# Performance work log

Measured on AMD Instinct MI355X. Metric: run time of the kernel, lower is better.

## Reference

```python
import jax, jax.numpy as jnp
import numpy as np

FEAT = 256
HEADS = 8
HD = FEAT // HEADS
POS = 128
NEG = 128
H = 128
W = 128
B = 8
NSLOT = 512
LN_EPS = 1e-5


def setup_inputs() -> dict:
    key = jax.random.key(0)
    ks = jax.random.split(key, 8)
    HW = H * W
    features = jax.random.normal(ks[0], (HW, B, FEAT), dtype=jnp.float32)
    pos_encodings = jax.random.normal(ks[1], (HW, B, FEAT), dtype=jnp.float32)
    slots = jax.random.normal(ks[2], (1, NSLOT, FEAT), dtype=jnp.float32)
    curio_maps = jax.random.uniform(ks[3], (NSLOT, H, W), dtype=jnp.float32)
    batch_idx = jax.random.randint(ks[4], (NSLOT,), 0, B, dtype=jnp.int32)
    # parameters (xavier-ish scale)
    in_proj_weight = jax.random.normal(ks[5], (3 * FEAT, FEAT), dtype=jnp.float32) * 0.05
    in_proj_bias = jnp.zeros((3 * FEAT,), dtype=jnp.float32)
    out_w = jax.random.normal(ks[6], (FEAT, FEAT), dtype=jnp.float32) * 0.05
    out_b = jnp.zeros((FEAT,), dtype=jnp.float32)
    ln_g = jnp.ones((FEAT,), dtype=jnp.float32)
    ln_b = jnp.zeros((FEAT,), dtype=jnp.float32)
    return {
        'slots': slots, 'features': features, 'pos_encodings': pos_encodings,
        'curio_maps': curio_maps, 'batch_idx': batch_idx,
        'in_proj_weight': in_proj_weight, 'in_proj_bias': in_proj_bias,
        'out_w': out_w, 'out_b': out_b, 'ln_g': ln_g, 'ln_b': ln_b,
        'max_mask_entries': 0,
    }


def _sample_feat_idx(curio_maps, max_mask_entries):
    # curio_maps: [NSLOT, H, W] -> feat_idx: [POS+NEG, NSLOT]
    HW = curio_maps.shape[1] * curio_maps.shape[2]
    flat = curio_maps.reshape(NSLOT, HW)
    sorted_idx = jnp.argsort(-flat, axis=1)  # descending
    pos_idx = sorted_idx[:, :POS]
    pool = sorted_idx[:, POS:HW - max_mask_entries] if max_mask_entries > 0 else sorted_idx[:, POS:]
    # deterministic stand-in for random.sample: evenly-strided negatives
    stride = pool.shape[1] // NEG
    neg_idx = pool[:, ::stride][:, :NEG]
    return jnp.concatenate([pos_idx, neg_idx], axis=1).T  # [S, NSLOT]


def _forward(slots, features, pos_encodings, curio_maps, batch_idx,
             in_proj_weight, in_proj_bias, out_w, out_b, ln_g, ln_b,
             max_mask_entries):
    feat_idx = _sample_feat_idx(curio_maps, max_mask_entries)  # [S, NSLOT]
    S = feat_idx.shape[0]
    qw, kw, vw = in_proj_weight[:FEAT], in_proj_weight[FEAT:2 * FEAT], in_proj_weight[2 * FEAT:]
    qb, kb, vb = in_proj_bias[:FEAT], in_proj_bias[FEAT:2 * FEAT], in_proj_bias[2 * FEAT:]
    scaling = float(HD) ** -0.5
    # sample_type == 'after': project full maps, then gather
    q = (jnp.einsum('bnf,gf->bng', slots, qw) + qb) * scaling       # [1, NSLOT, FEAT]
    k = jnp.einsum('pbf,gf->pbg', features + pos_encodings, kw) + kb  # [HW, B, FEAT]
    v = jnp.einsum('pbf,gf->pbg', features, vw) + vb                  # [HW, B, FEAT]
    kg = k[feat_idx, batch_idx[None, :], :]            # [S, NSLOT, FEAT]
    vg = v[feat_idx[:POS], batch_idx[None, :], :]      # [POS, NSLOT, FEAT]
    qh = q.reshape(NSLOT, HEADS, HD)
    kh = kg.reshape(S, NSLOT, HEADS, HD)
    vh = vg.reshape(POS, NSLOT, HEADS, HD)
    affinities = jnp.einsum('nhd,snhd->snh', qh, kh)   # [S, NSLOT, HEADS]
    attn = jax.nn.softmax(affinities[:POS], axis=0)    # softmax over positive samples
    attn_out = jnp.einsum('pnh,pnhd->nhd', attn, vh).reshape(1, NSLOT, FEAT)
    attn_out = jnp.einsum('bnf,gf->bng', attn_out, out_w) + out_b
    x = slots + attn_out  # dropout is identity in eval
    mu = jnp.mean(x, axis=-1, keepdims=True)
    var = jnp.var(x, axis=-1, keepdims=True)
    new_slots = (x - mu) / jnp.sqrt(var + LN_EPS) * ln_g + ln_b
    return new_slots, affinities


def reference(slots, features, pos_encodings, curio_maps, batch_idx,
              in_proj_weight, in_proj_bias, out_w, out_b, ln_g, ln_b,
              max_mask_entries):
    return _forward(slots, features, pos_encodings, curio_maps, batch_idx,
                    in_proj_weight, in_proj_bias, out_w, out_b, ln_g, ln_b,
                    max_mask_entries)
```

## Files before the change

kernel.cpp:

```cpp
#include <hip/hip_runtime.h>
#include <hip/hip_bf16.h>

#define FEAT 256
#define HEADS 8
#define HD 32
#define POSN 128
#define NEGN 128
#define HWN 16384
#define BN 8
#define NSLOT 512
#define S_TOT 256
#define LN_EPS 1e-5f
#define NBKT 4096
#define AFF_OFF (NSLOT*FEAT)

typedef float f32x4 __attribute__((ext_vector_type(4)));

__device__ __forceinline__ unsigned short bf16r(float x) {
    unsigned int u = __float_as_uint(x);
    u += 0x7FFFu + ((u >> 16) & 1u);
    return (unsigned short)(u >> 16);
}
__device__ __forceinline__ float bf16f(unsigned short h) {
    return __uint_as_float((unsigned int)h << 16);
}

__global__ __launch_bounds__(256) void k_sample_qkw(const float* __restrict__ curio,
                                                    const int* __restrict__ mme_p,
                                                    const float* __restrict__ slots,
                                                    const float* __restrict__ ipw,
                                                    const float* __restrict__ ipb,
                                                    int* __restrict__ fi_t,
                                                    float* __restrict__ qkw,
                                                    float* __restrict__ qkb)
{
    __shared__ unsigned int hist[NBKT];
    __shared__ uint16_t offs[NBKT];
    __shared__ uint16_t sidx[HWN];
    __shared__ unsigned int ssum[256];
    __shared__ float srow[FEAT];
    __shared__ float qrow[FEAT];
    int slot = blockIdx.x, t = threadIdx.x;
    const float* cm = curio + (size_t)slot * HWN;
    const f32x4* cm4 = (const f32x4*)cm;

    for (int i = t; i < NBKT; i += 256) hist[i] = 0;
    __syncthreads();

    unsigned int bkA[16], bkB[16];
#pragma unroll
    for (int j = 0; j < 16; j++) {
        f32x4 v = cm4[j * 256 + t];
        int b0 = (int)(v[0] * 4096.0f); b0 = b0 < 0 ? 0 : (b0 > NBKT-1 ? NBKT-1 : b0);
        int b1 = (int)(v[1] * 4096.0f); b1 = b1 < 0 ? 0 : (b1 > NBKT-1 ? NBKT-1 : b1);
        int b2 = (int)(v[2] * 4096.0f); b2 = b2 < 0 ? 0 : (b2 > NBKT-1 ? NBKT-1 : b2);
        int b3 = (int)(v[3] * 4096.0f); b3 = b3 < 0 ? 0 : (b3 > NBKT-1 ? NBKT-1 : b3);
        bkA[j] = (unsigned int)b0 | ((unsigned int)b1 << 16);
        bkB[j] = (unsigned int)b2 | ((unsigned int)b3 << 16);
        atomicAdd(&hist[b0], 1u); atomicAdd(&hist[b1], 1u);
        atomicAdd(&hist[b2], 1u); atomicAdd(&hist[b3], 1u);
    }
    __syncthreads();

    unsigned int lsum = 0;
    int base = t * 16;
    for (int j = 0; j < 16; j++) lsum += hist[NBKT-1 - (base + j)];
    ssum[t] = lsum; __syncthreads();
    for (int off = 1; off < 256; off <<= 1) {
        unsigned int v = (t >= off) ? ssum[t - off] : 0u;
        __syncthreads();
        ssum[t] += v;
        __syncthreads();
    }
    unsigned int run = ssum[t] - lsum;
    for (int j = 0; j < 16; j++) {
        int b = NBKT-1 - (base + j);
        offs[b] = (uint16_t)run;
        run += hist[b];
    }
    __syncthreads();
    for (int i = t; i < NBKT; i += 256) hist[i] = 0;
    __syncthreads();

#pragma unroll
    for (int j = 0; j < 16; j++) {
        int idx0 = (j * 256 + t) * 4;
        int b0 = (int)(bkA[j] & 0xFFFFu), b1 = (int)(bkA[j] >> 16);
        int b2 = (int)(bkB[j] & 0xFFFFu), b3 = (int)(bkB[j] >> 16);
        unsigned int p0 = (unsigned int)offs[b0] + atomicAdd(&hist[b0], 1u);
        sidx[p0] = (uint16_t)(idx0 + 0);
        unsigned int p1 = (unsigned int)offs[b1] + atomicAdd(&hist[b1], 1u);
        sidx[p1] = (uint16_t)(idx0 + 1);
        unsigned int p2 = (unsigned int)offs[b2] + atomicAdd(&hist[b2], 1u);
        sidx[p2] = (uint16_t)(idx0 + 2);
        unsigned int p3 = (unsigned int)offs[b3] + atomicAdd(&hist[b3], 1u);
        sidx[p3] = (uint16_t)(idx0 + 3);
    }
    __syncthreads();

    int mme = mme_p[0];
    int stride = (HWN - POSN - mme) / NEGN;
    int r = (t < POSN) ? t : (POSN + stride * (t - POSN));
    int lo = 0, hi = NBKT - 1;
    while (lo < hi) { int mid = (lo + hi) >> 1; if ((int)offs[mid] <= r) hi = mid; else lo = mid + 1; }
    int bkt = lo;
    int start = (int)offs[bkt];
    int cnt   = (int)hist[bkt];
    int rr = r - start;
    int besti = sidx[start + (rr < cnt ? rr : 0)];
    for (int j = 0; j < cnt; j++) {
        int ij = sidx[start + j];
        float vj = cm[ij];
        int rank = 0;
        for (int j2 = 0; j2 < cnt; j2++) {
            int i2 = sidx[start + j2];
            float v2 = cm[i2];
            if (v2 > vj || (v2 == vj && i2 < ij)) rank++;
        }
        if (rank == rr) { besti = ij; break; }
    }
    fi_t[slot * S_TOT + t] = besti;

    __syncthreads();
    srow[t] = slots[slot * FEAT + t];
    __syncthreads();
    {
        const float* qwrow = ipw + (size_t)t * FEAT;
        float acc = 0.f;
#pragma unroll 8
        for (int f = 0; f < FEAT; f++) acc += srow[f] * qwrow[f];
        const float scaling = 0.17677669529663687f;
        qrow[t] = (acc + ipb[t]) * scaling;
    }
    __syncthreads();
    if (t < HEADS) {
        float s = 0.f;
        for (int d = 0; d < HD; d++) s += qrow[t*HD + d] * ipb[FEAT + t*HD + d];
        qkb[slot * HEADS + t] = s;
    }
    const float* kw = ipw + FEAT * FEAT;
    for (int e = t; e < HEADS * FEAT; e += 256) {
        int h = e >> 8, f = e & 255;
        float s = 0.f;
#pragma unroll
        for (int d = 0; d < HD; d++) s += qrow[h*HD + d] * kw[(h*HD + d) * FEAT + f];
        qkw[(size_t)slot * (HEADS*FEAT) + e] = s;
    }
}

__global__ __launch_bounds__(512) void k_attn(const float* __restrict__ features,
                                              const float* __restrict__ pos_enc,
                                              const int* __restrict__ batch_idx,
                                              const int* __restrict__ fi_t,
                                              const float* __restrict__ qkw,
                                              const float* __restrict__ qkb,
                                              const float* __restrict__ slots,
                                              const float* __restrict__ ipw,
                                              const float* __restrict__ ipb,
                                              const float* __restrict__ out_w,
                                              const float* __restrict__ out_b,
                                              const float* __restrict__ ln_g,
                                              const float* __restrict__ ln_b,
                                              float* __restrict__ aff_out,
                                              float* __restrict__ out)
{
    __shared__ int   fi_l[S_TOT];
    __shared__ float qkb_l[HEADS];
    __shared__ __align__(16) float affP[POSN][8];
    __shared__ f32x4 wfp[4][HEADS][64];
    __shared__ f32x4 wf4[HEADS][64];
    __shared__ float aoh[512];
    __shared__ __align__(16) float ao_l[FEAT];
    __shared__ float xgh[512];
    __shared__ float r1[4], r2[4];

    int n = blockIdx.x, t = threadIdx.x, lane = t & 63, w = t >> 6;
    if (t < S_TOT) fi_l[t] = fi_t[n * S_TOT + t];
    if (t < HEADS) qkb_l[t] = qkb[n * HEADS + t];
    int b = batch_idx[n];

    const float* qk = qkw + (size_t)n * (HEADS*FEAT) + 4 * lane;
    f32x4 qw0 = *(const f32x4*)(qk + 0*FEAT);
    f32x4 qw1 = *(const f32x4*)(qk + 1*FEAT);
    f32x4 qw2 = *(const f32x4*)(qk + 2*FEAT);
    f32x4 qw3 = *(const f32x4*)(qk + 3*FEAT);
    f32x4 qw4 = *(const f32x4*)(qk + 4*FEAT);
    f32x4 qw5 = *(const f32x4*)(qk + 5*FEAT);
    f32x4 qw6 = *(const f32x4*)(qk + 6*FEAT);
    f32x4 qw7 = *(const f32x4*)(qk + 7*FEAT);
    __syncthreads();
    float qb = qkb_l[lane & 7];
    int b0 = lane & 1, b1 = (lane >> 1) & 1, b2 = (lane >> 2) & 1;

    auto dorow = [&](int p, f32x4 x, bool toLds) {
        float p0 = x[0]*qw0[0] + x[1]*qw0[1] + x[2]*qw0[2] + x[3]*qw0[3];
        float p1 = x[0]*qw1[0] + x[1]*qw1[1] + x[2]*qw1[2] + x[3]*qw1[3];
        float p2 = x[0]*qw2[0] + x[1]*qw2[1] + x[2]*qw2[2] + x[3]*qw2[3];
        float p3 = x[0]*qw3[0] + x[1]*qw3[1] + x[2]*qw3[2] + x[3]*qw3[3];
        float p4 = x[0]*qw4[0] + x[1]*qw4[1] + x[2]*qw4[2] + x[3]*qw4[3];
        float p5 = x[0]*qw5[0] + x[1]*qw5[1] + x[2]*qw5[2] + x[3]*qw5[3];
        float p6 = x[0]*qw6[0] + x[1]*qw6[1] + x[2]*qw6[2] + x[3]*qw6[3];
        float p7 = x[0]*qw7[0] + x[1]*qw7[1] + x[2]*qw7[2] + x[3]*qw7[3];
        float s0 = b0 ? p0 : p1, s1 = b0 ? p2 : p3, s2 = b0 ? p4 : p5, s3 = b0 ? p6 : p7;
        float a0 = (b0 ? p1 : p0) + __shfl_xor(s0, 1);
        float a1 = (b0 ? p3 : p2) + __shfl_xor(s1, 1);
        float a2 = (b0 ? p5 : p4) + __shfl_xor(s2, 1);
        float a3 = (b0 ? p7 : p6) + __shfl_xor(s3, 1);
        float u0 = b1 ? a0 : a1, u1 = b1 ? a2 : a3;
        float c0 = (b1 ? a1 : a0) + __shfl_xor(u0, 2);
        float c1 = (b1 ? a3 : a2) + __shfl_xor(u1, 2);
        float u2 = b2 ? c0 : c1;
        float d = (b2 ? c1 : c0) + __shfl_xor(u2, 4);
        d += __shfl_xor(d, 8);
        d += __shfl_xor(d, 16);
        d += __shfl_xor(d, 32);
        d += qb;
        if (lane < 8) {
            aff_out[(size_t)p * (NSLOT*HEADS) + n*HEADS + lane] = d;
            if (toLds) affP[p][lane] = d;
        }
    };

    auto rowaddr = [&](int s) {
        return ((size_t)fi_l[s] * BN + b) * FEAT + 4 * lane;
    };

    ushort4 cache[16];
    {
        size_t aA = rowaddr(w);
        size_t aB = rowaddr(w + 8);
        f32x4 fA = *(const f32x4*)(features + aA), gA = *(const f32x4*)(pos_enc + aA);
        f32x4 fB = *(const f32x4*)(features + aB), gB = *(const f32x4*)(pos_enc + aB);
#pragma unroll
        for (int i = 0; i < 16; i += 2) {
            f32x4 cf = fA, cg = gA;
            if (i + 2 < 16) {
                size_t nb = rowaddr(w + 8*(i+2));
                fA = *(const f32x4*)(features + nb); gA = *(const f32x4*)(pos_enc + nb);
            }
            { ushort4 pk; pk.x = bf16r(cf[0]); pk.y = bf16r(cf[1]);
              pk.z = bf16r(cf[2]); pk.w = bf16r(cf[3]); cache[i] = pk; }
            dorow(w + 8*i, cf + cg, true);
            f32x4 cf2 = fB, cg2 = gB;
            if (i + 3 < 16) {
                size_t nb = rowaddr(w + 8*(i+3));
                fB = *(const f32x4*)(features + nb); gB = *(const f32x4*)(pos_enc + nb);
            }
            { ushort4 pk; pk.x = bf16r(cf2[0]); pk.y = bf16r(cf2[1]);
              pk.z = bf16r(cf2[2]); pk.w = bf16r(cf2[3]); cache[i+1] = pk; }
            dorow(w + 8*(i+1), cf2 + cg2, true);
        }
    }
    __syncthreads();

    if (t < 256) {
        int h = t >> 5, l = t & 31;
        float v0 = affP[l][h], v1 = affP[l+32][h], v2 = affP[l+64][h], v3 = affP[l+96][h];
        float m = fmaxf(fmaxf(v0, v1), fmaxf(v2, v3));
        for (int off = 16; off > 0; off >>= 1) m = fmaxf(m, __shfl_xor(m, off, 32));
        float e0 = expf(v0 - m), e1 = expf(v1 - m), e2 = expf(v2 - m), e3 = expf(v3 - m);
        float s = e0 + e1 + e2 + e3;
        for (int off = 16; off > 0; off >>= 1) s += __shfl_xor(s, off, 32);
        float inv = 1.0f / s;
        affP[l][h] = e0*inv; affP[l+32][h] = e1*inv; affP[l+64][h] = e2*inv; affP[l+96][h] = e3*inv;
    }
    __syncthreads();

    f32x4 acc[8];
#pragma unroll
    for (int h = 0; h < 8; h++) acc[h] = (f32x4){0.f,0.f,0.f,0.f};
    {
        auto wstep = [&](int i) {
            int p = w + 8*i;
            ushort4 pk = cache[i];
            f32x4 xf;
            xf[0] = bf16f(pk.x); xf[1] = bf16f(pk.y);
            xf[2] = bf16f(pk.z); xf[3] = bf16f(pk.w);
            const f32x4* ap = (const f32x4*)&affP[p][0];
            f32x4 a03 = ap[0], a47 = ap[1];
            acc[0] += xf * a03[0];
            acc[1] += xf * a03[1];
            acc[2] += xf * a03[2];
            acc[3] += xf * a03[3];
            acc[4] += xf * a47[0];
            acc[5] += xf * a47[1];
            acc[6] += xf * a47[2];
            acc[7] += xf * a47[3];
        };
        size_t aA = rowaddr(POSN + w);
        size_t aB = rowaddr(POSN + w + 8);
        f32x4 fA = *(const f32x4*)(features + aA), gA = *(const f32x4*)(pos_enc + aA);
        f32x4 fB = *(const f32x4*)(features + aB), gB = *(const f32x4*)(pos_enc + aB);
#pragma unroll
        for (int i = 0; i < 16; i += 2) {
            f32x4 cf = fA, cg = gA;
            if (i + 2 < 16) {
                size_t nb = rowaddr(POSN + w + 8*(i+2));
                fA = *(const f32x4*)(features + nb); gA = *(const f32x4*)(pos_enc + nb);
            }
            wstep(i);
            dorow(POSN + w + 8*i, cf + cg, false);
            f32x4 cf2 = fB, cg2 = gB;
            if (i + 3 < 16) {
                size_t nb = rowaddr(POSN + w + 8*(i+3));
                fB = *(const f32x4*)(features + nb); gB = *(const f32x4*)(pos_enc + nb);
            }
            wstep(i+1);
            dorow(POSN + w + 8*(i+1), cf2 + cg2, false);
        }
    }
    if (w < 4) {
#pragma unroll
        for (int h = 0; h < 8; h++) wfp[w][h][lane] = acc[h];
    }
    __syncthreads();
    if (w >= 4) {
#pragma unroll
        for (int h = 0; h < 8; h++) wfp[w-4][h][lane] += acc[h];
    }
    __syncthreads();
    {
        int h = t >> 6, q2 = t & 63;
        f32x4 s = wfp[0][h][q2] + wfp[1][h][q2] + wfp[2][h][q2] + wfp[3][h][q2];
        wf4[h][q2] = s;
    }
    __syncthreads();

    {
        int g = t & 255, half = t >> 8;
        const float* vwrow = ipw + (size_t)(2*FEAT + g) * FEAT + half*128;
        const f32x4* wfv = &wf4[g >> 5][half*32];
        float s = 0.f;
#pragma unroll 8
        for (int f4i = 0; f4i < 32; f4i++) {
            f32x4 wv = *(const f32x4*)(vwrow + 4*f4i);
            f32x4 y = wfv[f4i];
            s += wv[0]*y[0] + wv[1]*y[1] + wv[2]*y[2] + wv[3]*y[3];
        }
        aoh[t] = s;
    }
    __syncthreads();
    if (t < 256) ao_l[t] = aoh[t] + aoh[t + 256] + ipb[2*FEAT + t];
    __syncthreads();

    {
        int g = t & 255, half = t >> 8;
        const float* owrow = out_w + (size_t)g * FEAT + half*128;
        const f32x4* av = (const f32x4*)&ao_l[half*128];
        float s = 0.f;
#pragma unroll 8
        for (int f4i = 0; f4i < 32; f4i++) {
            f32x4 wv = *(const f32x4*)(owrow + 4*f4i);
            f32x4 y = av[f4i];
            s += wv[0]*y[0] + wv[1]*y[1] + wv[2]*y[2] + wv[3]*y[3];
        }
        xgh[t] = s;
    }
    __syncthreads();

    float xg = 0.f;
    if (t < 256) {
        xg = xgh[t] + xgh[t + 256] + out_b[t] + slots[n * FEAT + t];
        float s1 = xg, s2 = xg * xg;
        for (int off = 32; off > 0; off >>= 1) {
            s1 += __shfl_xor(s1, off);
            s2 += __shfl_xor(s2, off);
        }
        if ((t & 63) == 0) { r1[t >> 6] = s1; r2[t >> 6] = s2; }
    }
    __syncthreads();
    if (t < 256) {
        float sum1 = r1[0] + r1[1] + r1[2] + r1[3];
        float sum2 = r2[0] + r2[1] + r2[2] + r2[3];
        float mu  = sum1 * (1.0f / FEAT);
        float var = sum2 * (1.0f / FEAT) - mu * mu;
        float nrm = (xg - mu) * rsqrtf(var + LN_EPS);
        out[n * FEAT + t] = nrm * ln_g[t] + ln_b[t];
    }
}

extern "C" void kernel_launch(void* const* d_in, const int* in_sizes, int n_in,
                              void* d_out, int out_size, void* d_ws, size_t ws_size,
                              hipStream_t stream)
{
    (void)in_sizes; (void)n_in; (void)out_size; (void)ws_size;
    const float* slots    = (const float*)d_in[0];
    const float* features = (const float*)d_in[1];
    const float* pos_enc  = (const float*)d_in[2];
    const float* curio    = (const float*)d_in[3];
    const int*   batch_idx= (const int*)d_in[4];
    const float* ipw      = (const float*)d_in[5];
    const float* ipb      = (const float*)d_in[6];
    const float* out_w    = (const float*)d_in[7];
    const float* out_b    = (const float*)d_in[8];
    const float* ln_g     = (const float*)d_in[9];
    const float* ln_b     = (const float*)d_in[10];
    const int*   mme      = (const int*)d_in[11];
    float* out = (float*)d_out;

    char* ws = (char*)d_ws;
    int*   fi_t = (int*)ws;
    float* qkw  = (float*)(ws + (512 << 10));
    float* qkb  = (float*)(ws + (512 << 10) + (4 << 20));
    float* aff  = out + AFF_OFF;

    hipLaunchKernelGGL(k_sample_qkw, dim3(NSLOT), dim3(256), 0, stream,
                       curio, mme, slots, ipw, ipb, fi_t, qkw, qkb);
    hipLaunchKernelGGL(k_attn, dim3(NSLOT), dim3(512), 0, stream,
                       features, pos_enc, batch_idx, fi_t, qkw, qkb, slots, ipw, ipb,
                       out_w, out_b, ln_g, ln_b, aff, out);
}
```

Measured before the change: 132.2 us.

## Split attention kernel into gather/reduce kernel and separate projection+LayerNorm kernel

```diff
diff --git a/kernel.cpp b/kernel.cpp
--- a/kernel.cpp
+++ b/kernel.cpp
@@ -148,31 +148,19 @@
     }
 }
 
-__global__ __launch_bounds__(512) void k_attn(const float* __restrict__ features,
-                                              const float* __restrict__ pos_enc,
-                                              const int* __restrict__ batch_idx,
-                                              const int* __restrict__ fi_t,
-                                              const float* __restrict__ qkw,
-                                              const float* __restrict__ qkb,
-                                              const float* __restrict__ slots,
-                                              const float* __restrict__ ipw,
-                                              const float* __restrict__ ipb,
-                                              const float* __restrict__ out_w,
-                                              const float* __restrict__ out_b,
-                                              const float* __restrict__ ln_g,
-                                              const float* __restrict__ ln_b,
-                                              float* __restrict__ aff_out,
-                                              float* __restrict__ out)
+__global__ __launch_bounds__(512) void k_attn_mem(const float* __restrict__ features,
+                                                  const float* __restrict__ pos_enc,
+                                                  const int* __restrict__ batch_idx,
+                                                  const int* __restrict__ fi_t,
+                                                  const float* __restrict__ qkw,
+                                                  const float* __restrict__ qkb,
+                                                  float* __restrict__ aff_out,
+                                                  f32x4* __restrict__ wf_g)
 {
     __shared__ int   fi_l[S_TOT];
     __shared__ float qkb_l[HEADS];
     __shared__ __align__(16) float affP[POSN][8];
     __shared__ f32x4 wfp[4][HEADS][64];
-    __shared__ f32x4 wf4[HEADS][64];
-    __shared__ float aoh[512];
-    __shared__ __align__(16) float ao_l[FEAT];
-    __shared__ float xgh[512];
-    __shared__ float r1[4], r2[4];
 
     int n = blockIdx.x, t = threadIdx.x, lane = t & 63, w = t >> 6;
     if (t < S_TOT) fi_l[t] = fi_t[n * S_TOT + t];
@@ -251,6 +239,14 @@
             dorow(w + 8*(i+1), cf2 + cg2, true);
         }
     }
+
+    f32x4 fA, gA, fB, gB;
+    {
+        size_t aA = rowaddr(POSN + w);
+        size_t aB = rowaddr(POSN + w + 8);
+        fA = *(const f32x4*)(features + aA); gA = *(const f32x4*)(pos_enc + aA);
+        fB = *(const f32x4*)(features + aB); gB = *(const f32x4*)(pos_enc + aB);
+    }
     __syncthreads();
 
     if (t < 256) {
@@ -287,10 +283,6 @@
             acc[6] += xf * a47[2];
             acc[7] += xf * a47[3];
         };
-        size_t aA = rowaddr(POSN + w);
-        size_t aB = rowaddr(POSN + w + 8);
-        f32x4 fA = *(const f32x4*)(features + aA), gA = *(const f32x4*)(pos_enc + aA);
-        f32x4 fB = *(const f32x4*)(features + aB), gB = *(const f32x4*)(pos_enc + aB);
 #pragma unroll
         for (int i = 0; i < 16; i += 2) {
             f32x4 cf = fA, cg = gA;
@@ -322,7 +314,30 @@
     {
         int h = t >> 6, q2 = t & 63;
         f32x4 s = wfp[0][h][q2] + wfp[1][h][q2] + wfp[2][h][q2] + wfp[3][h][q2];
-        wf4[h][q2] = s;
+        wf_g[(size_t)n * 512 + t] = s;
+    }
+}
+
+__global__ __launch_bounds__(512) void k_proj(const f32x4* __restrict__ wf_g,
+                                              const float* __restrict__ slots,
+                                              const float* __restrict__ ipw,
+                                              const float* __restrict__ ipb,
+                                              const float* __restrict__ out_w,
+                                              const float* __restrict__ out_b,
+                                              const float* __restrict__ ln_g,
+                                              const float* __restrict__ ln_b,
+                                              float* __restrict__ out)
+{
+    __shared__ f32x4 wf4[HEADS][64];
+    __shared__ float aoh[512];
+    __shared__ __align__(16) float ao_l[FEAT];
+    __shared__ float xgh[512];
+    __shared__ float r1[4], r2[4];
+
+    int n = blockIdx.x, t = threadIdx.x;
+    {
+        int h = t >> 6, q2 = t & 63;
+        wf4[h][q2] = wf_g[(size_t)n * 512 + t];
     }
     __syncthreads();
 
@@ -399,14 +414,19 @@
     float* out = (float*)d_out;
 
     char* ws = (char*)d_ws;
+    const size_t OFF_QKW = 512u << 10;
+    const size_t OFF_QKB = OFF_QKW + (4u << 20);
+    const size_t OFF_WF  = OFF_QKB + (64u << 10);
     int*   fi_t = (int*)ws;
-    float* qkw  = (float*)(ws + (512 << 10));
-    float* qkb  = (float*)(ws + (512 << 10) + (4 << 20));
+    float* qkw  = (float*)(ws + OFF_QKW);
+    float* qkb  = (float*)(ws + OFF_QKB);
+    f32x4* wf_g = (f32x4*)(ws + OFF_WF);
     float* aff  = out + AFF_OFF;
 
     hipLaunchKernelGGL(k_sample_qkw, dim3(NSLOT), dim3(256), 0, stream,
                        curio, mme, slots, ipw, ipb, fi_t, qkw, qkb);
-    hipLaunchKernelGGL(k_attn, dim3(NSLOT), dim3(512), 0, stream,
-                       features, pos_enc, batch_idx, fi_t, qkw, qkb, slots, ipw, ipb,
-                       out_w, out_b, ln_g, ln_b, aff, out);
-}
+    hipLaunchKernelGGL(k_attn_mem, dim3(NSLOT), dim3(512), 0, stream,
+                       features, pos_enc, batch_idx, fi_t, qkw, qkb, aff, wf_g);
+    hipLaunchKernelGGL(k_proj, dim3(NSLOT), dim3(512), 0, stream,
+                       wf_g, slots, ipw, ipb, out_w, out_b, ln_g, ln_b, out);
+}
```

After: 132.9 us. No clear change (+0.5%).

## Fuse sampling/QK-weight kernel into attention kernel with shared LDS union

Applied to the files above, without the earlier changes.

```diff
diff --git a/kernel.cpp b/kernel.cpp
--- a/kernel.cpp
+++ b/kernel.cpp
@@ -25,106 +25,129 @@
     return __uint_as_float((unsigned int)h << 16);
 }
 
-__global__ __launch_bounds__(256) void k_sample_qkw(const float* __restrict__ curio,
-                                                    const int* __restrict__ mme_p,
-                                                    const float* __restrict__ slots,
-                                                    const float* __restrict__ ipw,
-                                                    const float* __restrict__ ipb,
-                                                    int* __restrict__ fi_t,
-                                                    float* __restrict__ qkw,
-                                                    float* __restrict__ qkb)
+__global__ __launch_bounds__(512) void k_fused(const float* __restrict__ curio,
+                                               const int* __restrict__ mme_p,
+                                               const float* __restrict__ slots,
+                                               const float* __restrict__ ipw,
+                                               const float* __restrict__ ipb,
+                                               const int* __restrict__ batch_idx,
+                                               const float* __restrict__ features,
+                                               const float* __restrict__ pos_enc,
+                                               const float* __restrict__ out_w,
+                                               const float* __restrict__ out_b,
+                                               const float* __restrict__ ln_g,
+                                               const float* __restrict__ ln_b,
+                                               float* __restrict__ aff_out,
+                                               float* __restrict__ out)
 {
-    __shared__ unsigned int hist[NBKT];
-    __shared__ uint16_t offs[NBKT];
-    __shared__ uint16_t sidx[HWN];
-    __shared__ unsigned int ssum[256];
+    __shared__ __align__(16) char U[59392];
+    unsigned int* hist = (unsigned int*)U;
+    uint16_t*     offs = (uint16_t*)(U + 16384);
+    uint16_t*     sidx = (uint16_t*)(U + 24576);
+    unsigned int* ssum = (unsigned int*)(U + 57344);
+    float (*affP)[8] = (float(*)[8])U;
+    f32x4 (*wfp)[HEADS][64] = (f32x4(*)[HEADS][64])(U + 4096);
+    f32x4 (*wf4)[64] = (f32x4(*)[64])(U + 36864);
+    float* aoh  = (float*)(U + 45056);
+    float* ao_l = (float*)(U + 47104);
+    float* xgh  = (float*)(U + 48128);
+    float* rr12 = (float*)(U + 50176);
+    __shared__ int   fi_l[S_TOT];
+    __shared__ float qkwL[HEADS*FEAT];
+    __shared__ float qkb_l[HEADS];
     __shared__ float srow[FEAT];
     __shared__ float qrow[FEAT];
-    int slot = blockIdx.x, t = threadIdx.x;
-    const float* cm = curio + (size_t)slot * HWN;
+
+    int n = blockIdx.x, t = threadIdx.x, lane = t & 63, w = t >> 6;
+    const float* cm = curio + (size_t)n * HWN;
     const f32x4* cm4 = (const f32x4*)cm;
-
-    for (int i = t; i < NBKT; i += 256) hist[i] = 0;
-    __syncthreads();
-
-    unsigned int bkA[16], bkB[16];
-#pragma unroll
-    for (int j = 0; j < 16; j++) {
-        f32x4 v = cm4[j * 256 + t];
-        int b0 = (int)(v[0] * 4096.0f); b0 = b0 < 0 ? 0 : (b0 > NBKT-1 ? NBKT-1 : b0);
-        int b1 = (int)(v[1] * 4096.0f); b1 = b1 < 0 ? 0 : (b1 > NBKT-1 ? NBKT-1 : b1);
-        int b2 = (int)(v[2] * 4096.0f); b2 = b2 < 0 ? 0 : (b2 > NBKT-1 ? NBKT-1 : b2);
-        int b3 = (int)(v[3] * 4096.0f); b3 = b3 < 0 ? 0 : (b3 > NBKT-1 ? NBKT-1 : b3);
-        bkA[j] = (unsigned int)b0 | ((unsigned int)b1 << 16);
-        bkB[j] = (unsigned int)b2 | ((unsigned int)b3 << 16);
-        atomicAdd(&hist[b0], 1u); atomicAdd(&hist[b1], 1u);
-        atomicAdd(&hist[b2], 1u); atomicAdd(&hist[b3], 1u);
-    }
-    __syncthreads();
-
-    unsigned int lsum = 0;
-    int base = t * 16;
-    for (int j = 0; j < 16; j++) lsum += hist[NBKT-1 - (base + j)];
-    ssum[t] = lsum; __syncthreads();
-    for (int off = 1; off < 256; off <<= 1) {
-        unsigned int v = (t >= off) ? ssum[t - off] : 0u;
-        __syncthreads();
-        ssum[t] += v;
-        __syncthreads();
-    }
-    unsigned int run = ssum[t] - lsum;
-    for (int j = 0; j < 16; j++) {
-        int b = NBKT-1 - (base + j);
-        offs[b] = (uint16_t)run;
-        run += hist[b];
-    }
-    __syncthreads();
-    for (int i = t; i < NBKT; i += 256) hist[i] = 0;
-    __syncthreads();
-
-#pragma unroll
-    for (int j = 0; j < 16; j++) {
-        int idx0 = (j * 256 + t) * 4;
-        int b0 = (int)(bkA[j] & 0xFFFFu), b1 = (int)(bkA[j] >> 16);
-        int b2 = (int)(bkB[j] & 0xFFFFu), b3 = (int)(bkB[j] >> 16);
-        unsigned int p0 = (unsigned int)offs[b0] + atomicAdd(&hist[b0], 1u);
+    int b = batch_idx[n];
+
+    for (int i = t; i < NBKT; i += 512) hist[i] = 0;
+    __syncthreads();
+
+    unsigned int bkA[8], bkB[8];
+#pragma unroll
+    for (int j = 0; j < 8; j++) {
+        f32x4 v = cm4[j * 512 + t];
+        int c0 = (int)(v[0] * 4096.0f); c0 = c0 < 0 ? 0 : (c0 > NBKT-1 ? NBKT-1 : c0);
+        int c1 = (int)(v[1] * 4096.0f); c1 = c1 < 0 ? 0 : (c1 > NBKT-1 ? NBKT-1 : c1);
+        int c2 = (int)(v[2] * 4096.0f); c2 = c2 < 0 ? 0 : (c2 > NBKT-1 ? NBKT-1 : c2);
+        int c3 = (int)(v[3] * 4096.0f); c3 = c3 < 0 ? 0 : (c3 > NBKT-1 ? NBKT-1 : c3);
+        bkA[j] = (unsigned int)c0 | ((unsigned int)c1 << 16);
+        bkB[j] = (unsigned int)c2 | ((unsigned int)c3 << 16);
+        atomicAdd(&hist[c0], 1u); atomicAdd(&hist[c1], 1u);
+        atomicAdd(&hist[c2], 1u); atomicAdd(&hist[c3], 1u);
+    }
+    __syncthreads();
+
+    {
+        unsigned int lsum = 0;
+        int base = t * 8;
+        for (int j = 0; j < 8; j++) lsum += hist[NBKT-1 - (base + j)];
+        ssum[t] = lsum; __syncthreads();
+        for (int off = 1; off < 512; off <<= 1) {
+            unsigned int v = (t >= off) ? ssum[t - off] : 0u;
+            __syncthreads();
+            ssum[t] += v;
+            __syncthreads();
+        }
+        unsigned int run = ssum[t] - lsum;
+        for (int j = 0; j < 8; j++) {
+            int bb = NBKT-1 - (base + j);
+            offs[bb] = (uint16_t)run;
+            run += hist[bb];
+        }
+    }
+    __syncthreads();
+    for (int i = t; i < NBKT; i += 512) hist[i] = 0;
+    __syncthreads();
+
+#pragma unroll
+    for (int j = 0; j < 8; j++) {
+        int idx0 = (j * 512 + t) * 4;
+        int c0 = (int)(bkA[j] & 0xFFFFu), c1 = (int)(bkA[j] >> 16);
+        int c2 = (int)(bkB[j] & 0xFFFFu), c3 = (int)(bkB[j] >> 16);
+        unsigned int p0 = (unsigned int)offs[c0] + atomicAdd(&hist[c0], 1u);
         sidx[p0] = (uint16_t)(idx0 + 0);
-        unsigned int p1 = (unsigned int)offs[b1] + atomicAdd(&hist[b1], 1u);
+        unsigned int p1 = (unsigned int)offs[c1] + atomicAdd(&hist[c1], 1u);
         sidx[p1] = (uint16_t)(idx0 + 1);
-        unsigned int p2 = (unsigned int)offs[b2] + atomicAdd(&hist[b2], 1u);
+        unsigned int p2 = (unsigned int)offs[c2] + atomicAdd(&hist[c2], 1u);
         sidx[p2] = (uint16_t)(idx0 + 2);
-        unsigned int p3 = (unsigned int)offs[b3] + atomicAdd(&hist[b3], 1u);
+        unsigned int p3 = (unsigned int)offs[c3] + atomicAdd(&hist[c3], 1u);
         sidx[p3] = (uint16_t)(idx0 + 3);
     }
     __syncthreads();
 
-    int mme = mme_p[0];
-    int stride = (HWN - POSN - mme) / NEGN;
-    int r = (t < POSN) ? t : (POSN + stride * (t - POSN));
-    int lo = 0, hi = NBKT - 1;
-    while (lo < hi) { int mid = (lo + hi) >> 1; if ((int)offs[mid] <= r) hi = mid; else lo = mid + 1; }
-    int bkt = lo;
-    int start = (int)offs[bkt];
-    int cnt   = (int)hist[bkt];
-    int rr = r - start;
-    int besti = sidx[start + (rr < cnt ? rr : 0)];
-    for (int j = 0; j < cnt; j++) {
-        int ij = sidx[start + j];
-        float vj = cm[ij];
-        int rank = 0;
-        for (int j2 = 0; j2 < cnt; j2++) {
-            int i2 = sidx[start + j2];
-            float v2 = cm[i2];
-            if (v2 > vj || (v2 == vj && i2 < ij)) rank++;
-        }
-        if (rank == rr) { besti = ij; break; }
-    }
-    fi_t[slot * S_TOT + t] = besti;
-
-    __syncthreads();
-    srow[t] = slots[slot * FEAT + t];
-    __syncthreads();
-    {
+    if (t < S_TOT) {
+        int mme = mme_p[0];
+        int stride = (HWN - POSN - mme) / NEGN;
+        int r = (t < POSN) ? t : (POSN + stride * (t - POSN));
+        int lo = 0, hi = NBKT - 1;
+        while (lo < hi) { int mid = (lo + hi) >> 1; if ((int)offs[mid] <= r) hi = mid; else lo = mid + 1; }
+        int bkt = lo;
+        int start = (int)offs[bkt];
+        int cnt   = (int)hist[bkt];
+        int rsel  = r - start;
+        int besti = sidx[start + (rsel < cnt ? rsel : 0)];
+        for (int j = 0; j < cnt; j++) {
+            int ij = sidx[start + j];
+            float vj = cm[ij];
+            int rank = 0;
+            for (int j2 = 0; j2 < cnt; j2++) {
+                int i2 = sidx[start + j2];
+                float v2 = cm[i2];
+                if (v2 > vj || (v2 == vj && i2 < ij)) rank++;
+            }
+            if (rank == rsel) { besti = ij; break; }
+        }
+        fi_l[t] = besti;
+    }
+
+    __syncthreads();
+    if (t < FEAT) srow[t] = slots[n * FEAT + t];
+    __syncthreads();
+    if (t < FEAT) {
         const float* qwrow = ipw + (size_t)t * FEAT;
         float acc = 0.f;
 #pragma unroll 8
@@ -136,61 +159,30 @@
     if (t < HEADS) {
         float s = 0.f;
         for (int d = 0; d < HD; d++) s += qrow[t*HD + d] * ipb[FEAT + t*HD + d];
-        qkb[slot * HEADS + t] = s;
-    }
-    const float* kw = ipw + FEAT * FEAT;
-    for (int e = t; e < HEADS * FEAT; e += 256) {
-        int h = e >> 8, f = e & 255;
-        float s = 0.f;
-#pragma unroll
-        for (int d = 0; d < HD; d++) s += qrow[h*HD + d] * kw[(h*HD + d) * FEAT + f];
-        qkw[(size_t)slot * (HEADS*FEAT) + e] = s;
-    }
-}
-
-__global__ __launch_bounds__(512) void k_attn(const float* __restrict__ features,
-                                              const float* __restrict__ pos_enc,
-                                              const int* __restrict__ batch_idx,
-                                              const int* __restrict__ fi_t,
-                                              const float* __restrict__ qkw,
-                                              const float* __restrict__ qkb,
-                                              const float* __restrict__ slots,
-                                              const float* __restrict__ ipw,
-                                              const float* __restrict__ ipb,
-                                              const float* __restrict__ out_w,
-                                              const float* __restrict__ out_b,
-                                              const float* __restrict__ ln_g,
-                                              const float* __restrict__ ln_b,
-                                              float* __restrict__ aff_out,
-                                              float* __restrict__ out)
-{
-    __shared__ int   fi_l[S_TOT];
-    __shared__ float qkb_l[HEADS];
-    __shared__ __align__(16) float affP[POSN][8];
-    __shared__ f32x4 wfp[4][HEADS][64];
-    __shared__ f32x4 wf4[HEADS][64];
-    __shared__ float aoh[512];
-    __shared__ __align__(16) float ao_l[FEAT];
-    __shared__ float xgh[512];
-    __shared__ float r1[4], r2[4];
-
-    int n = blockIdx.x, t = threadIdx.x, lane = t & 63, w = t >> 6;
-    if (t < S_TOT) fi_l[t] = fi_t[n * S_TOT + t];
-    if (t < HEADS) qkb_l[t] = qkb[n * HEADS + t];
-    int b = batch_idx[n];
-
-    const float* qk = qkw + (size_t)n * (HEADS*FEAT) + 4 * lane;
-    f32x4 qw0 = *(const f32x4*)(qk + 0*FEAT);
-    f32x4 qw1 = *(const f32x4*)(qk + 1*FEAT);
-    f32x4 qw2 = *(const f32x4*)(qk + 2*FEAT);
-    f32x4 qw3 = *(const f32x4*)(qk + 3*FEAT);
-    f32x4 qw4 = *(const f32x4*)(qk + 4*FEAT);
-    f32x4 qw5 = *(const f32x4*)(qk + 5*FEAT);
-    f32x4 qw6 = *(const f32x4*)(qk + 6*FEAT);
-    f32x4 qw7 = *(const f32x4*)(qk + 7*FEAT);
-    __syncthreads();
+        qkb_l[t] = s;
+    }
+    {
+        const float* kw = ipw + FEAT * FEAT;
+        for (int e = t; e < HEADS * FEAT; e += 512) {
+            int h = e >> 8, f = e & 255;
+            float s = 0.f;
+#pragma unroll
+            for (int d = 0; d < HD; d++) s += qrow[h*HD + d] * kw[(h*HD + d) * FEAT + f];
+            qkwL[e] = s;
+        }
+    }
+    __syncthreads();
+
+    f32x4 qw0 = *(const f32x4*)&qkwL[0*FEAT + 4*lane];
+    f32x4 qw1 = *(const f32x4*)&qkwL[1*FEAT + 4*lane];
+    f32x4 qw2 = *(const f32x4*)&qkwL[2*FEAT + 4*lane];
+    f32x4 qw3 = *(const f32x4*)&qkwL[3*FEAT + 4*lane];
+    f32x4 qw4 = *(const f32x4*)&qkwL[4*FEAT + 4*lane];
+    f32x4 qw5 = *(const f32x4*)&qkwL[5*FEAT + 4*lane];
+    f32x4 qw6 = *(const f32x4*)&qkwL[6*FEAT + 4*lane];
+    f32x4 qw7 = *(const f32x4*)&qkwL[7*FEAT + 4*lane];
     float qb = qkb_l[lane & 7];
-    int b0 = lane & 1, b1 = (lane >> 1) & 1, b2 = (lane >> 2) & 1;
+    int e0 = lane & 1, e1 = (lane >> 1) & 1, e2 = (lane >> 2) & 1;
 
     auto dorow = [&](int p, f32x4 x, bool toLds) {
         float p0 = x[0]*qw0[0] + x[1]*qw0[1] + x[2]*qw0[2] + x[3]*qw0[3];
@@ -201,16 +193,16 @@
         float p5 = x[0]*qw5[0] + x[1]*qw5[1] + x[2]*qw5[2] + x[3]*qw5[3];
         float p6 = x[0]*qw6[0] + x[1]*qw6[1] + x[2]*qw6[2] + x[3]*qw6[3];
         float p7 = x[0]*qw7[0] + x[1]*qw7[1] + x[2]*qw7[2] + x[3]*qw7[3];
-        float s0 = b0 ? p0 : p1, s1 = b0 ? p2 : p3, s2 = b0 ? p4 : p5, s3 = b0 ? p6 : p7;
-        float a0 = (b0 ? p1 : p0) + __shfl_xor(s0, 1);
-        float a1 = (b0 ? p3 : p2) + __shfl_xor(s1, 1);
-        float a2 = (b0 ? p5 : p4) + __shfl_xor(s2, 1);
-        float a3 = (b0 ? p7 : p6) + __shfl_xor(s3, 1);
-        float u0 = b1 ? a0 : a1, u1 = b1 ? a2 : a3;
-        float c0 = (b1 ? a1 : a0) + __shfl_xor(u0, 2);
-        float c1 = (b1 ? a3 : a2) + __shfl_xor(u1, 2);
-        float u2 = b2 ? c0 : c1;
-        float d = (b2 ? c1 : c0) + __shfl_xor(u2, 4);
+        float s0 = e0 ? p0 : p1, s1 = e0 ? p2 : p3, s2 = e0 ? p4 : p5, s3 = e0 ? p6 : p7;
+        float a0 = (e0 ? p1 : p0) + __shfl_xor(s0, 1);
+        float a1 = (e0 ? p3 : p2) + __shfl_xor(s1, 1);
+        float a2 = (e0 ? p5 : p4) + __shfl_xor(s2, 1);
+        float a3 = (e0 ? p7 : p6) + __shfl_xor(s3, 1);
+        float u0 = e1 ? a0 : a1, u1 = e1 ? a2 : a3;
+        float c0 = (e1 ? a1 : a0) + __shfl_xor(u0, 2);
+        float c1 = (e1 ? a3 : a2) + __shfl_xor(u1, 2);
+        float u2 = e2 ? c0 : c1;
+        float d = (e2 ? c1 : c0) + __shfl_xor(u2, 4);
         d += __shfl_xor(d, 8);
         d += __shfl_xor(d, 16);
         d += __shfl_xor(d, 32);
@@ -251,6 +243,14 @@
             dorow(w + 8*(i+1), cf2 + cg2, true);
         }
     }
+
+    f32x4 fA, gA, fB, gB;
+    {
+        size_t aA = rowaddr(POSN + w);
+        size_t aB = rowaddr(POSN + w + 8);
+        fA = *(const f32x4*)(features + aA); gA = *(const f32x4*)(pos_enc + aA);
+        fB = *(const f32x4*)(features + aB); gB = *(const f32x4*)(pos_enc + aB);
+    }
     __syncthreads();
 
     if (t < 256) {
@@ -258,11 +258,11 @@
         float v0 = affP[l][h], v1 = affP[l+32][h], v2 = affP[l+64][h], v3 = affP[l+96][h];
         float m = fmaxf(fmaxf(v0, v1), fmaxf(v2, v3));
         for (int off = 16; off > 0; off >>= 1) m = fmaxf(m, __shfl_xor(m, off, 32));
-        float e0 = expf(v0 - m), e1 = expf(v1 - m), e2 = expf(v2 - m), e3 = expf(v3 - m);
-        float s = e0 + e1 + e2 + e3;
+        float ex0 = expf(v0 - m), ex1 = expf(v1 - m), ex2 = expf(v2 - m), ex3 = expf(v3 - m);
+        float s = ex0 + ex1 + ex2 + ex3;
         for (int off = 16; off > 0; off >>= 1) s += __shfl_xor(s, off, 32);
         float inv = 1.0f / s;
-        affP[l][h] = e0*inv; affP[l+32][h] = e1*inv; affP[l+64][h] = e2*inv; affP[l+96][h] = e3*inv;
+        affP[l][h] = ex0*inv; affP[l+32][h] = ex1*inv; affP[l+64][h] = ex2*inv; affP[l+96][h] = ex3*inv;
     }
     __syncthreads();
 
@@ -287,10 +287,6 @@
             acc[6] += xf * a47[2];
             acc[7] += xf * a47[3];
         };
-        size_t aA = rowaddr(POSN + w);
-        size_t aB = rowaddr(POSN + w + 8);
-        f32x4 fA = *(const f32x4*)(features + aA), gA = *(const f32x4*)(pos_enc + aA);
-        f32x4 fB = *(const f32x4*)(features + aB), gB = *(const f32x4*)(pos_enc + aB);
 #pragma unroll
         for (int i = 0; i < 16; i += 2) {
             f32x4 cf = fA, cg = gA;
@@ -321,8 +317,7 @@
     __syncthreads();
     {
         int h = t >> 6, q2 = t & 63;
-        f32x4 s = wfp[0][h][q2] + wfp[1][h][q2] + wfp[2][h][q2] + wfp[3][h][q2];
-        wf4[h][q2] = s;
+        wf4[h][q2] = wfp[0][h][q2] + wfp[1][h][q2] + wfp[2][h][q2] + wfp[3][h][q2];
     }
     __syncthreads();
 
@@ -342,7 +337,6 @@
     __syncthreads();
     if (t < 256) ao_l[t] = aoh[t] + aoh[t + 256] + ipb[2*FEAT + t];
     __syncthreads();
-
     {
         int g = t & 255, half = t >> 8;
         const float* owrow = out_w + (size_t)g * FEAT + half*128;
@@ -366,12 +360,12 @@
             s1 += __shfl_xor(s1, off);
             s2 += __shfl_xor(s2, off);
         }
-        if ((t & 63) == 0) { r1[t >> 6] = s1; r2[t >> 6] = s2; }
+        if ((t & 63) == 0) { rr12[t >> 6] = s1; rr12[4 + (t >> 6)] = s2; }
     }
     __syncthreads();
     if (t < 256) {
-        float sum1 = r1[0] + r1[1] + r1[2] + r1[3];
-        float sum2 = r2[0] + r2[1] + r2[2] + r2[3];
+        float sum1 = rr12[0] + rr12[1] + rr12[2] + rr12[3];
+        float sum2 = rr12[4] + rr12[5] + rr12[6] + rr12[7];
         float mu  = sum1 * (1.0f / FEAT);
         float var = sum2 * (1.0f / FEAT) - mu * mu;
         float nrm = (xg - mu) * rsqrtf(var + LN_EPS);
@@ -383,7 +377,7 @@
                               void* d_out, int out_size, void* d_ws, size_t ws_size,
                               hipStream_t stream)
 {
-    (void)in_sizes; (void)n_in; (void)out_size; (void)ws_size;
+    (void)in_sizes; (void)n_in; (void)out_size; (void)d_ws; (void)ws_size;
     const float* slots    = (const float*)d_in[0];
     const float* features = (const float*)d_in[1];
     const float* pos_enc  = (const float*)d_in[2];
@@ -397,16 +391,9 @@
     const float* ln_b     = (const float*)d_in[10];
     const int*   mme      = (const int*)d_in[11];
     float* out = (float*)d_out;
-
-    char* ws = (char*)d_ws;
-    int*   fi_t = (int*)ws;
-    float* qkw  = (float*)(ws + (512 << 10));
-    float* qkb  = (float*)(ws + (512 << 10) + (4 << 20));
-    float* aff  = out + AFF_OFF;
-
-    hipLaunchKernelGGL(k_sample_qkw, dim3(NSLOT), dim3(256), 0, stream,
-                       curio, mme, slots, ipw, ipb, fi_t, qkw, qkb);
-    hipLaunchKernelGGL(k_attn, dim3(NSLOT), dim3(512), 0, stream,
-                       features, pos_enc, batch_idx, fi_t, qkw, qkb, slots, ipw, ipb,
+    float* aff = out + AFF_OFF;
+
+    hipLaunchKernelGGL(k_fused, dim3(NSLOT), dim3(512), 0, stream,
+                       curio, mme, slots, ipw, ipb, batch_idx, features, pos_enc,
                        out_w, out_b, ln_g, ln_b, aff, out);
 }
```

Result: slower. 140.5 us (+6.2%).

## Coalesce matvecs via wave-cooperative dot8w and prefetch negative rows before softmax

Applied to the files above, without the earlier changes.

```diff
diff --git a/kernel.cpp b/kernel.cpp
--- a/kernel.cpp
+++ b/kernel.cpp
@@ -23,6 +23,42 @@
 }
 __device__ __forceinline__ float bf16f(unsigned short h) {
     return __uint_as_float((unsigned int)h << 16);
+}
+
+__device__ __forceinline__ float dot8w(const float* __restrict__ Wrows,
+                                       f32x4 x, int e0, int e1, int e2, int lane)
+{
+    const float* p = Wrows + 4 * lane;
+    f32x4 w0 = *(const f32x4*)(p + 0*FEAT);
+    f32x4 w1 = *(const f32x4*)(p + 1*FEAT);
+    f32x4 w2 = *(const f32x4*)(p + 2*FEAT);
+    f32x4 w3 = *(const f32x4*)(p + 3*FEAT);
+    f32x4 w4 = *(const f32x4*)(p + 4*FEAT);
+    f32x4 w5 = *(const f32x4*)(p + 5*FEAT);
+    f32x4 w6 = *(const f32x4*)(p + 6*FEAT);
+    f32x4 w7 = *(const f32x4*)(p + 7*FEAT);
+    float p0 = x[0]*w0[0] + x[1]*w0[1] + x[2]*w0[2] + x[3]*w0[3];
+    float p1 = x[0]*w1[0] + x[1]*w1[1] + x[2]*w1[2] + x[3]*w1[3];
+    float p2 = x[0]*w2[0] + x[1]*w2[1] + x[2]*w2[2] + x[3]*w2[3];
+    float p3 = x[0]*w3[0] + x[1]*w3[1] + x[2]*w3[2] + x[3]*w3[3];
+    float p4 = x[0]*w4[0] + x[1]*w4[1] + x[2]*w4[2] + x[3]*w4[3];
+    float p5 = x[0]*w5[0] + x[1]*w5[1] + x[2]*w5[2] + x[3]*w5[3];
+    float p6 = x[0]*w6[0] + x[1]*w6[1] + x[2]*w6[2] + x[3]*w6[3];
+    float p7 = x[0]*w7[0] + x[1]*w7[1] + x[2]*w7[2] + x[3]*w7[3];
+    float s0 = e0 ? p0 : p1, s1 = e0 ? p2 : p3, s2 = e0 ? p4 : p5, s3 = e0 ? p6 : p7;
+    float a0 = (e0 ? p1 : p0) + __shfl_xor(s0, 1);
+    float a1 = (e0 ? p3 : p2) + __shfl_xor(s1, 1);
+    float a2 = (e0 ? p5 : p4) + __shfl_xor(s2, 1);
+    float a3 = (e0 ? p7 : p6) + __shfl_xor(s3, 1);
+    float u0 = e1 ? a0 : a1, u1 = e1 ? a2 : a3;
+    float c0 = (e1 ? a1 : a0) + __shfl_xor(u0, 2);
+    float c1 = (e1 ? a3 : a2) + __shfl_xor(u1, 2);
+    float u2 = e2 ? c0 : c1;
+    float d = (e2 ? c1 : c0) + __shfl_xor(u2, 4);
+    d += __shfl_xor(d, 8);
+    d += __shfl_xor(d, 16);
+    d += __shfl_xor(d, 32);
+    return d;
 }
 
 __global__ __launch_bounds__(256) void k_sample_qkw(const float* __restrict__ curio,
@@ -41,6 +77,7 @@
     __shared__ float srow[FEAT];
     __shared__ float qrow[FEAT];
     int slot = blockIdx.x, t = threadIdx.x;
+    int lane = t & 63, w = t >> 6;
     const float* cm = curio + (size_t)slot * HWN;
     const f32x4* cm4 = (const f32x4*)cm;
 
@@ -125,12 +162,15 @@
     srow[t] = slots[slot * FEAT + t];
     __syncthreads();
     {
-        const float* qwrow = ipw + (size_t)t * FEAT;
-        float acc = 0.f;
-#pragma unroll 8
-        for (int f = 0; f < FEAT; f++) acc += srow[f] * qwrow[f];
+        int e0 = lane & 1, e1 = (lane >> 1) & 1, e2 = (lane >> 2) & 1;
+        f32x4 xs = *(const f32x4*)&srow[4 * lane];
         const float scaling = 0.17677669529663687f;
-        qrow[t] = (acc + ipb[t]) * scaling;
+#pragma unroll
+        for (int c = 0; c < 8; c++) {
+            int r0 = w * 64 + c * 8;
+            float d = dot8w(ipw + (size_t)r0 * FEAT, xs, e0, e1, e2, lane);
+            if (lane < 8) qrow[r0 + lane] = (d + ipb[r0 + lane]) * scaling;
+        }
     }
     __syncthreads();
     if (t < HEADS) {
@@ -168,11 +208,9 @@
     __shared__ float qkb_l[HEADS];
     __shared__ __align__(16) float affP[POSN][8];
     __shared__ f32x4 wfp[4][HEADS][64];
-    __shared__ f32x4 wf4[HEADS][64];
-    __shared__ float aoh[512];
     __shared__ __align__(16) float ao_l[FEAT];
-    __shared__ float xgh[512];
-    __shared__ float r1[4], r2[4];
+    __shared__ float xgh[FEAT];
+    __shared__ float rr12[8];
 
     int n = blockIdx.x, t = threadIdx.x, lane = t & 63, w = t >> 6;
     if (t < S_TOT) fi_l[t] = fi_t[n * S_TOT + t];
@@ -190,7 +228,7 @@
     f32x4 qw7 = *(const f32x4*)(qk + 7*FEAT);
     __syncthreads();
     float qb = qkb_l[lane & 7];
-    int b0 = lane & 1, b1 = (lane >> 1) & 1, b2 = (lane >> 2) & 1;
+    int e0 = lane & 1, e1 = (lane >> 1) & 1, e2 = (lane >> 2) & 1;
 
     auto dorow = [&](int p, f32x4 x, bool toLds) {
         float p0 = x[0]*qw0[0] + x[1]*qw0[1] + x[2]*qw0[2] + x[3]*qw0[3];
@@ -201,16 +239,16 @@
         float p5 = x[0]*qw5[0] + x[1]*qw5[1] + x[2]*qw5[2] + x[3]*qw5[3];
         float p6 = x[0]*qw6[0] + x[1]*qw6[1] + x[2]*qw6[2] + x[3]*qw6[3];
         float p7 = x[0]*qw7[0] + x[1]*qw7[1] + x[2]*qw7[2] + x[3]*qw7[3];
-        float s0 = b0 ? p0 : p1, s1 = b0 ? p2 : p3, s2 = b0 ? p4 : p5, s3 = b0 ? p6 : p7;
-        float a0 = (b0 ? p1 : p0) + __shfl_xor(s0, 1);
-        float a1 = (b0 ? p3 : p2) + __shfl_xor(s1, 1);
-        float a2 = (b0 ? p5 : p4) + __shfl_xor(s2, 1);
-        float a3 = (b0 ? p7 : p6) + __shfl_xor(s3, 1);
-        float u0 = b1 ? a0 : a1, u1 = b1 ? a2 : a3;
-        float c0 = (b1 ? a1 : a0) + __shfl_xor(u0, 2);
-        float c1 = (b1 ? a3 : a2) + __shfl_xor(u1, 2);
-        float u2 = b2 ? c0 : c1;
-        float d = (b2 ? c1 : c0) + __shfl_xor(u2, 4);
+        float s0 = e0 ? p0 : p1, s1 = e0 ? p2 : p3, s2 = e0 ? p4 : p5, s3 = e0 ? p6 : p7;
+        float a0 = (e0 ? p1 : p0) + __shfl_xor(s0, 1);
+        float a1 = (e0 ? p3 : p2) + __shfl_xor(s1, 1);
+        float a2 = (e0 ? p5 : p4) + __shfl_xor(s2, 1);
+        float a3 = (e0 ? p7 : p6) + __shfl_xor(s3, 1);
+        float u0 = e1 ? a0 : a1, u1 = e1 ? a2 : a3;
+        float c0 = (e1 ? a1 : a0) + __shfl_xor(u0, 2);
+        float c1 = (e1 ? a3 : a2) + __shfl_xor(u1, 2);
+        float u2 = e2 ? c0 : c1;
+        float d = (e2 ? c1 : c0) + __shfl_xor(u2, 4);
         d += __shfl_xor(d, 8);
         d += __shfl_xor(d, 16);
         d += __shfl_xor(d, 32);
@@ -251,6 +289,14 @@
             dorow(w + 8*(i+1), cf2 + cg2, true);
         }
     }
+
+    f32x4 fA, gA, fB, gB;
+    {
+        size_t aA = rowaddr(POSN + w);
+        size_t aB = rowaddr(POSN + w + 8);
+        fA = *(const f32x4*)(features + aA); gA = *(const f32x4*)(pos_enc + aA);
+        fB = *(const f32x4*)(features + aB); gB = *(const f32x4*)(pos_enc + aB);
+    }
     __syncthreads();
 
     if (t < 256) {
@@ -258,11 +304,11 @@
         float v0 = affP[l][h], v1 = affP[l+32][h], v2 = affP[l+64][h], v3 = affP[l+96][h];
         float m = fmaxf(fmaxf(v0, v1), fmaxf(v2, v3));
         for (int off = 16; off > 0; off >>= 1) m = fmaxf(m, __shfl_xor(m, off, 32));
-        float e0 = expf(v0 - m), e1 = expf(v1 - m), e2 = expf(v2 - m), e3 = expf(v3 - m);
-        float s = e0 + e1 + e2 + e3;
+        float ex0 = expf(v0 - m), ex1 = expf(v1 - m), ex2 = expf(v2 - m), ex3 = expf(v3 - m);
+        float s = ex0 + ex1 + ex2 + ex3;
         for (int off = 16; off > 0; off >>= 1) s += __shfl_xor(s, off, 32);
         float inv = 1.0f / s;
-        affP[l][h] = e0*inv; affP[l+32][h] = e1*inv; affP[l+64][h] = e2*inv; affP[l+96][h] = e3*inv;
+        affP[l][h] = ex0*inv; affP[l+32][h] = ex1*inv; affP[l+64][h] = ex2*inv; affP[l+96][h] = ex3*inv;
     }
     __syncthreads();
 
@@ -287,10 +333,6 @@
             acc[6] += xf * a47[2];
             acc[7] += xf * a47[3];
         };
-        size_t aA = rowaddr(POSN + w);
-        size_t aB = rowaddr(POSN + w + 8);
-        f32x4 fA = *(const f32x4*)(features + aA), gA = *(const f32x4*)(pos_enc + aA);
-        f32x4 fB = *(const f32x4*)(features + aB), gB = *(const f32x4*)(pos_enc + aB);
 #pragma unroll
         for (int i = 0; i < 16; i += 2) {
             f32x4 cf = fA, cg = gA;
@@ -322,56 +364,47 @@
     {
         int h = t >> 6, q2 = t & 63;
         f32x4 s = wfp[0][h][q2] + wfp[1][h][q2] + wfp[2][h][q2] + wfp[3][h][q2];
-        wf4[h][q2] = s;
-    }
-    __syncthreads();
-
-    {
-        int g = t & 255, half = t >> 8;
-        const float* vwrow = ipw + (size_t)(2*FEAT + g) * FEAT + half*128;
-        const f32x4* wfv = &wf4[g >> 5][half*32];
-        float s = 0.f;
-#pragma unroll 8
-        for (int f4i = 0; f4i < 32; f4i++) {
-            f32x4 wv = *(const f32x4*)(vwrow + 4*f4i);
-            f32x4 y = wfv[f4i];
-            s += wv[0]*y[0] + wv[1]*y[1] + wv[2]*y[2] + wv[3]*y[3];
-        }
-        aoh[t] = s;
-    }
-    __syncthreads();
-    if (t < 256) ao_l[t] = aoh[t] + aoh[t + 256] + ipb[2*FEAT + t];
-    __syncthreads();
-
-    {
-        int g = t & 255, half = t >> 8;
-        const float* owrow = out_w + (size_t)g * FEAT + half*128;
-        const f32x4* av = (const f32x4*)&ao_l[half*128];
-        float s = 0.f;
-#pragma unroll 8
-        for (int f4i = 0; f4i < 32; f4i++) {
-            f32x4 wv = *(const f32x4*)(owrow + 4*f4i);
-            f32x4 y = av[f4i];
-            s += wv[0]*y[0] + wv[1]*y[1] + wv[2]*y[2] + wv[3]*y[3];
-        }
-        xgh[t] = s;
+        wfp[0][h][q2] = s;
+    }
+    __syncthreads();
+
+    {
+        const float* vw = ipw + (size_t)(2*FEAT) * FEAT;
+        f32x4 xv = wfp[0][w][lane];
+#pragma unroll
+        for (int c = 0; c < 4; c++) {
+            int r0 = w * 32 + c * 8;
+            float d = dot8w(vw + (size_t)r0 * FEAT, xv, e0, e1, e2, lane);
+            if (lane < 8) ao_l[r0 + lane] = d + ipb[2*FEAT + r0 + lane];
+        }
+    }
+    __syncthreads();
+
+    {
+        f32x4 xo = *(const f32x4*)&ao_l[4 * lane];
+#pragma unroll
+        for (int c = 0; c < 4; c++) {
+            int r0 = w * 32 + c * 8;
+            float d = dot8w(out_w + (size_t)r0 * FEAT, xo, e0, e1, e2, lane);
+            if (lane < 8) xgh[r0 + lane] = d;
+        }
     }
     __syncthreads();
 
     float xg = 0.f;
     if (t < 256) {
-        xg = xgh[t] + xgh[t + 256] + out_b[t] + slots[n * FEAT + t];
+        xg = xgh[t] + out_b[t] + slots[n * FEAT + t];
         float s1 = xg, s2 = xg * xg;
         for (int off = 32; off > 0; off >>= 1) {
             s1 += __shfl_xor(s1, off);
             s2 += __shfl_xor(s2, off);
         }
-        if ((t & 63) == 0) { r1[t >> 6] = s1; r2[t >> 6] = s2; }
+        if ((t & 63) == 0) { rr12[t >> 6] = s1; rr12[4 + (t >> 6)] = s2; }
     }
     __syncthreads();
     if (t < 256) {
-        float sum1 = r1[0] + r1[1] + r1[2] + r1[3];
-        float sum2 = r2[0] + r2[1] + r2[2] + r2[3];
+        float sum1 = rr12[0] + rr12[1] + rr12[2] + rr12[3];
+        float sum2 = rr12[4] + rr12[5] + rr12[6] + rr12[7];
         float mu  = sum1 * (1.0f / FEAT);
         float var = sum2 * (1.0f / FEAT) - mu * mu;
         float nrm = (xg - mu) * rsqrtf(var + LN_EPS);
```

Result: faster. 109.5 us (-17.1%).
